# Kernel optimization log

Hardware: AMD Instinct MI355X
Metric: run time of the kernel (lower is better)

Reference implementation:

```python
import jax, jax.numpy as jnp
import numpy as np

B, T, O, H, CTX, HOR = 32, 24, 128, 512, 256, 48
MAX_STEP = 2.0


def setup_inputs() -> dict:
    key = jax.random.key(0)
    ks = jax.random.split(key, 20)
    def lin(k, out_d, in_d):
        bound = 1.0 / np.sqrt(in_d)
        kw, kb = jax.random.split(k)
        W = jax.random.uniform(kw, (out_d, in_d), jnp.float32, -bound, bound)
        b = jax.random.uniform(kb, (out_d,), jnp.float32, -bound, bound)
        return W, b
    W_emb, b_emb = lin(ks[0], H, 2)
    W_ctx, b_ctx = lin(ks[1], H, CTX)
    Wi_enc, bi_enc = lin(ks[2], 3 * H, H)
    Wh_enc, bh_enc = lin(ks[3], 3 * H, H)
    Wi_cell, bi_cell = lin(ks[4], 3 * H, H)
    Wh_cell, bh_cell = lin(ks[5], 3 * H, H)
    W1, b1 = lin(ks[6], H, H)
    W2, b2 = lin(ks[7], 2, H)
    z_ctx = jax.random.normal(ks[8], (B, CTX), jnp.float32)
    traj_hist = jax.random.uniform(ks[9], (B, T, O, 2), jnp.float32) * 10.0
    return dict(z_ctx=z_ctx, traj_hist=traj_hist,
                W_emb=W_emb, b_emb=b_emb, W_ctx=W_ctx, b_ctx=b_ctx,
                Wi_enc=Wi_enc, Wh_enc=Wh_enc, bi_enc=bi_enc, bh_enc=bh_enc,
                Wi_cell=Wi_cell, Wh_cell=Wh_cell, bi_cell=bi_cell, bh_cell=bh_cell,
                W1=W1, b1=b1, W2=W2, b2=b2, horizon=HOR)


def _gru(h, x, Wi, Wh, bi, bh):
    # PyTorch GRU gate math: gates ordered (r, z, n)
    gi = x @ Wi.T + bi  # [N, 3H]
    gh = h @ Wh.T + bh
    ir, iz, inn = jnp.split(gi, 3, axis=-1)
    hr, hz, hn = jnp.split(gh, 3, axis=-1)
    r = jax.nn.sigmoid(ir + hr)
    z = jax.nn.sigmoid(iz + hz)
    n = jnp.tanh(inn + r * hn)
    return (1.0 - z) * n + z * h


def reference(z_ctx, traj_hist, W_emb, b_emb, W_ctx, b_ctx,
              Wi_enc, Wh_enc, bi_enc, bh_enc,
              Wi_cell, Wh_cell, bi_cell, bh_cell,
              W1, b1, W2, b2, horizon):
    b, t, o, _ = traj_hist.shape
    Hd = W_emb.shape[0]
    seq = traj_hist.transpose(0, 2, 1, 3).reshape(b * o, t, 2)  # [N, t, 2]
    emb = seq @ W_emb.T + b_emb  # [N, t, H]

    h0 = jnp.zeros((b * o, Hd), traj_hist.dtype)
    def enc_step(h, x):
        return _gru(h, x, Wi_enc, Wh_enc, bi_enc, bh_enc), None
    h, _ = jax.lax.scan(enc_step, h0, emb.transpose(1, 0, 2))

    ctx = z_ctx @ W_ctx.T + b_ctx                         # [b, H]
    ctx = jnp.repeat(ctx[:, None, :], o, axis=1).reshape(b * o, Hd)
    h = h + ctx

    state0 = seq[:, -1]  # [N, 2]
    def dec_step(carry, _):
        h, state = carry
        inp = state @ W_emb.T + b_emb
        h = _gru(h, inp, Wi_cell, Wh_cell, bi_cell, bh_cell)
        d = jax.nn.gelu(h @ W1.T + b1, approximate=False) @ W2.T + b2  # [N, 2]
        d = MAX_STEP * jnp.tanh(d / MAX_STEP)
        s = state + d
        state = jnp.stack([jnp.clip(s[..., 0], -90.0, 90.0),
                           jnp.mod(s[..., 1], 360.0)], axis=-1)
        return (h, state), state
    _, outs = jax.lax.scan(dec_step, (h, state0), None, length=horizon)
    # outs: [horizon, N, 2] -> [b, horizon, o, 2]
    return outs.transpose(1, 0, 2).reshape(b, o, horizon, 2).transpose(0, 2, 1, 3)
```

## Files before the change

kernel.cpp:

```cpp
#include <hip/hip_runtime.h>
#include <hip/hip_bf16.h>
#include <math.h>

#define BB 32
#define TT 24
#define OO 128
#define HH 512
#define CTXD 256
#define HOR 48
#define NN (BB*OO)
#define G3 (3*HH)
#define KS2 16
#define TILE_U16 (KS2*512)

typedef unsigned short ushortt;
typedef __attribute__((ext_vector_type(8))) short bf16x8;
typedef __attribute__((ext_vector_type(4))) float f32x4;

__device__ __forceinline__ ushortt f2bf(float x) {
    union { float f; unsigned u; } v; v.f = x;
    unsigned r = v.u + 0x7FFF + ((v.u >> 16) & 1);
    return (ushortt)(r >> 16);
}
__device__ __forceinline__ float bf2f(ushortt b) {
    union { unsigned u; float f; } v; v.u = ((unsigned)b) << 16;
    return v.f;
}
__device__ __forceinline__ void splitbf(float x, ushortt& hi, ushortt& lo) {
    hi = f2bf(x);
    lo = f2bf(x - bf2f(hi));
}
__device__ __forceinline__ float sigm(float x) { return 1.f / (1.f + __expf(-x)); }
__device__ __forceinline__ float tanh_fast(float x) {
    float xc = fminf(fmaxf(x, -10.f), 10.f);
    float e = __expf(2.f * xc);
    return (e - 1.f) / (e + 1.f);
}

__device__ __forceinline__ void group_barrier(unsigned* cnt, unsigned target) {
    __syncthreads();
    if (threadIdx.x == 0) {
        __hip_atomic_fetch_add(cnt, 1u, __ATOMIC_RELAXED, __HIP_MEMORY_SCOPE_AGENT);
        while (__hip_atomic_load(cnt, __ATOMIC_RELAXED, __HIP_MEMORY_SCOPE_AGENT) < target)
            __builtin_amdgcn_s_sleep(2);
    }
    __syncthreads();
    asm volatile("buffer_inv sc0\n\ts_waitcnt vmcnt(0)" ::: "memory");
}


#define MLOADA(Ad, ksv) do { const unsigned ko = (unsigned)(ksv) * 512; \
  _Pragma("unroll") for (int m_ = 0; m_ < 2; m_++) { \
    Ad[m_*2+0] = *reinterpret_cast<const bf16x8*>(RAh + ao[m_] + ko); \
    Ad[m_*2+1] = *reinterpret_cast<const bf16x8*>(RAl + ao[m_] + ko); \
  } } while(0)
#define MLOADB(Bd, ksv) do { const unsigned ko = (unsigned)(ksv) * 512; \
  _Pragma("unroll") for (int g_ = 0; g_ < 3; g_++) { \
    Bd[g_*2+0] = *reinterpret_cast<const bf16x8*>(Bh + bo[g_] + ko); \
    Bd[g_*2+1] = *reinterpret_cast<const bf16x8*>(Bl + bo[g_] + ko); \
  } } while(0)
#define MMFMA(Av, Bv) do { \
  _Pragma("unroll") for (int m_ = 0; m_ < 2; m_++) \
  _Pragma("unroll") for (int g_ = 0; g_ < 3; g_++) \
    acc[m_][g_] = __builtin_amdgcn_mfma_f32_16x16x32_bf16(Av[m_*2+0], Bv[g_*2+0], acc[m_][g_], 0,0,0); \
  _Pragma("unroll") for (int m_ = 0; m_ < 2; m_++) \
  _Pragma("unroll") for (int g_ = 0; g_ < 3; g_++) \
    acc[m_][g_] = __builtin_amdgcn_mfma_f32_16x16x32_bf16(Av[m_*2+0], Bv[g_*2+1], acc[m_][g_], 0,0,0); \
  _Pragma("unroll") for (int m_ = 0; m_ < 2; m_++) \
  _Pragma("unroll") for (int g_ = 0; g_ < 3; g_++) \
    acc[m_][g_] = __builtin_amdgcn_mfma_f32_16x16x32_bf16(Av[m_*2+1], Bv[g_*2+0], acc[m_][g_], 0,0,0); \
  } while(0)

#define HLOADA(Ad, ksv) do { const unsigned ko = (unsigned)(ksv) * 512; \
  _Pragma("unroll") for (int m_ = 0; m_ < 2; m_++) { \
    Ad[m_*2+0] = *reinterpret_cast<const bf16x8*>(WAh + ao[m_] + ko); \
    Ad[m_*2+1] = *reinterpret_cast<const bf16x8*>(WAl + ao[m_] + ko); \
  } } while(0)
#define HLOADB(Bd, ksv) do { const unsigned ko = (unsigned)(ksv) * 512; \
    Bd[0] = *reinterpret_cast<const bf16x8*>(W1H + bo1 + ko); \
    Bd[1] = *reinterpret_cast<const bf16x8*>(W1L + bo1 + ko); \
  } while(0)
#define HMFMA(Av, Bv) do { \
  _Pragma("unroll") for (int m_ = 0; m_ < 2; m_++) { \
    hacc[m_] = __builtin_amdgcn_mfma_f32_16x16x32_bf16(Av[m_*2+0], Bv[0], hacc[m_], 0,0,0); \
    hacc[m_] = __builtin_amdgcn_mfma_f32_16x16x32_bf16(Av[m_*2+0], Bv[1], hacc[m_], 0,0,0); \
    hacc[m_] = __builtin_amdgcn_mfma_f32_16x16x32_bf16(Av[m_*2+1], Bv[0], hacc[m_], 0,0,0); \
  } } while(0)

__global__ __launch_bounds__(256, 4) void main_kernel(
    ushortt* Ah0, ushortt* Al0, ushortt* Ah1, ushortt* Al1,
    const ushortt* __restrict__ WheH, const ushortt* __restrict__ WheL,
    const ushortt* __restrict__ WhdH, const ushortt* __restrict__ WhdL,
    const ushortt* __restrict__ W1H,  const ushortt* __restrict__ W1L,
    const float* __restrict__ Ue, const float* __restrict__ ce,
    const float* __restrict__ Ud, const float* __restrict__ cd,
    const float* __restrict__ bhe, const float* __restrict__ bhd,
    const float* __restrict__ traj, const float* __restrict__ ctx,
    const float* __restrict__ b1v, const float* __restrict__ W2,
    const float* __restrict__ b2v, float* __restrict__ dpart,
    unsigned* bar, float* __restrict__ out)
{
    __shared__ float hbuf[128 * 20];
    __shared__ float sstate[128 * 2];
    const int mb = blockIdx.x & 31;
    const int jb = blockIdx.x >> 5;
    const int w = threadIdx.x >> 6, lane = threadIdx.x & 63;
    const int quad = lane >> 4, l15 = lane & 15;
    const int mtg = mb * 8 + w * 2;
    const int jlo = jb * 16;
    const int jcol = jlo + l15;
    unsigned* grpcnt = bar + mb * 16;
    unsigned tgt = 0;

    ushortt* bh_[2] = {Ah0, Ah1};
    ushortt* bl_[2] = {Al0, Al1};

    unsigned ao[2], bo[3], bo1;
#pragma unroll
    for (int mt = 0; mt < 2; mt++) ao[mt] = (unsigned)(mtg + mt) * TILE_U16 + lane * 8;
#pragma unroll
    for (int g = 0; g < 3; g++) bo[g] = (unsigned)(g*32 + jb) * TILE_U16 + lane * 8;
    bo1 = (unsigned)jb * TILE_U16 + lane * 8;

    const float b1r = b1v[jcol], w2a = W2[jcol], w2b = W2[HH + jcol];
    const float b20 = b2v[0], b21 = b2v[1];

    float Ur0, Ur1, Uz0, Uz1, Un0, Un1, Crr, Czz, bhn, cinn;

#pragma unroll 1
    for (int s = 0; s < TT + HOR; s++) {
        const bool enc = s < TT;
        if (s == 0 || s == TT) {
            const float* U  = enc ? Ue : Ud;
            const float* ci = enc ? ce : cd;
            const float* bh = enc ? bhe : bhd;
            Ur0 = U[jcol*2];            Ur1 = U[jcol*2+1];
            Uz0 = U[(512+jcol)*2];      Uz1 = U[(512+jcol)*2+1];
            Un0 = U[(1024+jcol)*2];     Un1 = U[(1024+jcol)*2+1];
            Crr = ci[jcol] + bh[jcol];
            Czz = ci[512+jcol] + bh[512+jcol];
            cinn = ci[1024+jcol];       bhn = bh[1024+jcol];
            if (!enc) {
                if (threadIdx.x < 128) {
                    int lrow = threadIdx.x;
                    const float* sp = traj + (((size_t)mb * TT + 23) * OO + lrow) * 2;
                    sstate[lrow*2] = sp[0]; sstate[lrow*2+1] = sp[1];
                }
                __syncthreads();
            }
        }
        const ushortt* RAh = bh_[s & 1];
        const ushortt* RAl = bl_[s & 1];
        ushortt* WAh = bh_[(s + 1) & 1];
        ushortt* WAl = bl_[(s + 1) & 1];
        const ushortt* Bh = enc ? WheH : WhdH;
        const ushortt* Bl = enc ? WheL : WhdL;

        f32x4 acc[2][3];
#pragma unroll
        for (int a = 0; a < 2; a++)
#pragma unroll
            for (int g = 0; g < 3; g++) acc[a][g] = (f32x4){0.f,0.f,0.f,0.f};

        if (s > 0) {
            bf16x8 aC[4], bC[6], aN[4], bN[6];
            MLOADA(aC, 0); MLOADB(bC, 0);
#pragma unroll 1
            for (int ks = 0; ks < 14; ks += 2) {
                MLOADA(aN, ks+1); MLOADB(bN, ks+1);
                MMFMA(aC, bC);
                MLOADA(aC, ks+2); MLOADB(bC, ks+2);
                MMFMA(aN, bN);
            }
            MLOADA(aN, 15); MLOADB(bN, 15);
            MMFMA(aC, bC);
            MMFMA(aN, bN);
        }

        float x0v[2][4], x1v[2][4];
#pragma unroll
        for (int mt = 0; mt < 2; mt++)
#pragma unroll
            for (int reg = 0; reg < 4; reg++) {
                int lrow = (w*2 + mt) * 16 + quad * 4 + reg;
                if (enc) {
                    const float* p = traj + (((size_t)mb * TT + s) * OO + lrow) * 2;
                    x0v[mt][reg] = p[0]; x1v[mt][reg] = p[1];
                } else {
                    x0v[mt][reg] = sstate[lrow*2]; x1v[mt][reg] = sstate[lrow*2+1];
                }
            }

#pragma unroll
        for (int mt = 0; mt < 2; mt++)
#pragma unroll
            for (int reg = 0; reg < 4; reg++) {
                int lrow = (w*2 + mt) * 16 + quad * 4 + reg;
                float x0 = x0v[mt][reg], x1 = x1v[mt][reg];
                float pr = acc[mt][0][reg] + fmaf(x1, Ur1, fmaf(x0, Ur0, Crr));
                float pz = acc[mt][1][reg] + fmaf(x1, Uz1, fmaf(x0, Uz0, Czz));
                float hn = acc[mt][2][reg] + bhn;
                float inn = fmaf(x1, Un1, fmaf(x0, Un0, cinn));
                float hold = (s > 0) ? hbuf[lrow * 20 + l15] : 0.f;
                float rg = sigm(pr), zg = sigm(pz);
                float nn = tanh_fast(inn + rg * hn);
                float h = (1.f - zg) * nn + zg * hold;
                if (enc && s == TT - 1)
                    h += ctx[(size_t)mb * HH + jcol];
                hbuf[lrow * 20 + l15] = h;
            }
        __syncthreads();
        {
            int fr = threadIdx.x;
            int mt8 = fr >> 5, rem = fr & 31;
            int qk = rem >> 4, r15 = rem & 15;
            const float4 v0 = *reinterpret_cast<const float4*>(&hbuf[(mt8*16 + r15) * 20 + qk * 8]);
            const float4 v1 = *reinterpret_cast<const float4*>(&hbuf[(mt8*16 + r15) * 20 + qk * 8 + 4]);
            float src[8] = {v0.x, v0.y, v0.z, v0.w, v1.x, v1.y, v1.z, v1.w};
            bf16x8 hv, lv;
#pragma unroll
            for (int q = 0; q < 8; q++) {
                ushortt hi, lo; splitbf(src[q], hi, lo);
                hv[q] = (short)hi; lv[q] = (short)lo;
            }
            int quadg = (jb & 1) * 2 + qk;
            unsigned base = (unsigned)(mb*8 + mt8) * TILE_U16 + (unsigned)(jb >> 1) * 512
                          + (unsigned)(quadg * 16 + r15) * 8;
            *reinterpret_cast<bf16x8*>(WAh + base) = hv;
            *reinterpret_cast<bf16x8*>(WAl + base) = lv;
        }

        tgt += 32;
        group_barrier(grpcnt, tgt);

        if (!enc) {
            f32x4 hacc[2];
            hacc[0] = (f32x4){0.f,0.f,0.f,0.f};
            hacc[1] = (f32x4){0.f,0.f,0.f,0.f};
            {
                bf16x8 aC[4], bC[2], aN[4], bN[2];
                HLOADA(aC, 0); HLOADB(bC, 0);
#pragma unroll 1
                for (int ks = 0; ks < 14; ks += 2) {
                    HLOADA(aN, ks+1); HLOADB(bN, ks+1);
                    HMFMA(aC, bC);
                    HLOADA(aC, ks+2); HLOADB(bC, ks+2);
                    HMFMA(aN, bN);
                }
                HLOADA(aN, 15); HLOADB(bN, 15);
                HMFMA(aC, bC);
                HMFMA(aN, bN);
            }
            float p0[2][4], p1[2][4];
#pragma unroll
            for (int mt = 0; mt < 2; mt++)
#pragma unroll
                for (int reg = 0; reg < 4; reg++) {
                    float v = hacc[mt][reg] + b1r;
                    v = 0.5f * v * (1.0f + erff(v * 0.70710678118654752440f));
                    p0[mt][reg] = v * w2a;
                    p1[mt][reg] = v * w2b;
                }
#pragma unroll
            for (int m = 1; m < 16; m <<= 1)
#pragma unroll
                for (int mt = 0; mt < 2; mt++)
#pragma unroll
                    for (int reg = 0; reg < 4; reg++) {
                        p0[mt][reg] += __shfl_xor(p0[mt][reg], m, 64);
                        p1[mt][reg] += __shfl_xor(p1[mt][reg], m, 64);
                    }
            if (l15 == 0) {
#pragma unroll
                for (int mt = 0; mt < 2; mt++)
#pragma unroll
                    for (int reg = 0; reg < 4; reg++) {
                        int lrow = (w*2 + mt) * 16 + quad * 4 + reg;
                        float* dp = dpart + ((size_t)(mb*32 + jb) * 128 + lrow) * 2;
                        dp[0] = p0[mt][reg]; dp[1] = p1[mt][reg];
                    }
            }
            tgt += 32;
            group_barrier(grpcnt, tgt);
            if (threadIdx.x < 128) {
                int lrow = threadIdx.x;
                float d0 = 0.f, d1 = 0.f;
#pragma unroll 8
                for (int j2 = 0; j2 < 32; j2++) {
                    const float* dp = dpart + ((size_t)(mb*32 + j2) * 128 + lrow) * 2;
                    d0 += dp[0]; d1 += dp[1];
                }
                d0 += b20; d1 += b21;
                d0 = 2.0f * tanhf(d0 * 0.5f);
                d1 = 2.0f * tanhf(d1 * 0.5f);
                float s0 = sstate[lrow*2] + d0;
                s0 = fminf(fmaxf(s0, -90.f), 90.f);
                float s1 = sstate[lrow*2+1] + d1;
                float rrm = fmodf(s1, 360.f);
                if (rrm < 0.f) rrm += 360.f;
                sstate[lrow*2] = s0; sstate[lrow*2+1] = rrm;
                if (jb == 0) {
                    float* op = out + (((size_t)mb * HOR + (s - TT)) * OO + lrow) * 2;
                    op[0] = s0; op[1] = rrm;
                }
            }
            __syncthreads();
        }
    }
}

__device__ __forceinline__ void pack16(const float* __restrict__ W,
                                       ushortt* __restrict__ Fh, ushortt* __restrict__ Fl,
                                       int item) {
    int n = item >> 6, rem = item & 63;
    int ks = rem >> 2, quadk = rem & 3;
    int nt = n >> 4, l15 = n & 15;
    ushortt hv[8], lv[8];
#pragma unroll
    for (int q = 0; q < 8; q++) {
        float v = W[(size_t)n * 512 + ks*32 + quadk*8 + q];
        ushortt hi, lo; splitbf(v, hi, lo);
        hv[q] = hi; lv[q] = lo;
    }
    size_t pos = ((size_t)nt * TILE_U16) + (size_t)ks * 512 + (quadk*16 + l15) * 8;
#pragma unroll
    for (int q = 0; q < 8; q++) { Fh[pos + q] = hv[q]; Fl[pos + q] = lv[q]; }
}

__global__ __launch_bounds__(256) void prep_kernel(
    const float* __restrict__ Wh_enc, const float* __restrict__ Wh_cell,
    const float* __restrict__ W1,
    const float* __restrict__ Wi_enc, const float* __restrict__ bi_enc,
    const float* __restrict__ Wi_cell, const float* __restrict__ bi_cell,
    const float* __restrict__ W_emb, const float* __restrict__ b_emb,
    const float* __restrict__ z, const float* __restrict__ Wc, const float* __restrict__ bc,
    ushortt* __restrict__ WheH, ushortt* __restrict__ WheL,
    ushortt* __restrict__ WhdH, ushortt* __restrict__ WhdL,
    ushortt* __restrict__ W1H, ushortt* __restrict__ W1L,
    float* __restrict__ Ue, float* __restrict__ ce,
    float* __restrict__ Ud, float* __restrict__ cd,
    float* __restrict__ ctx, unsigned* __restrict__ bar)
{
    int b = blockIdx.x;
    if (b < 384) {
        pack16(Wh_enc, WheH, WheL, b * 256 + threadIdx.x);
    } else if (b < 768) {
        pack16(Wh_cell, WhdH, WhdL, (b - 384) * 256 + threadIdx.x);
    } else if (b < 896) {
        pack16(W1, W1H, W1L, (b - 768) * 256 + threadIdx.x);
    } else if (b < 1664) {
        int w = threadIdx.x >> 6, lane = threadIdx.x & 63;
        int gidx = (b - 896) * 4 + w;
        int which = gidx >= G3;
        int j = gidx - which * G3;
        const float* Wi = which ? Wi_cell : Wi_enc;
        const float* bi = which ? bi_cell : bi_enc;
        float u0 = 0.f, u1 = 0.f, cc = 0.f;
#pragma unroll
        for (int i = 0; i < 8; i++) {
            int k = i * 64 + lane;
            float wv = Wi[(size_t)j * HH + k];
            u0 = fmaf(wv, W_emb[2*k],   u0);
            u1 = fmaf(wv, W_emb[2*k+1], u1);
            cc = fmaf(wv, b_emb[k],     cc);
        }
#pragma unroll
        for (int m = 1; m < 64; m <<= 1) {
            u0 += __shfl_xor(u0, m, 64);
            u1 += __shfl_xor(u1, m, 64);
            cc += __shfl_xor(cc, m, 64);
        }
        if (lane == 0) {
            float* Uo = which ? Ud : Ue;
            float* cv = which ? cd : ce;
            Uo[j*2] = u0; Uo[j*2+1] = u1; cv[j] = cc + bi[j];
        }
    } else if (b < 1728) {
        int idx = (b - 1664) * 256 + threadIdx.x;
        int bb = idx >> 9, j = idx & 511;
        float acc = bc[j];
        const float4* zp = (const float4*)(z + (size_t)bb * CTXD);
        const float4* wp = (const float4*)(Wc + (size_t)j * CTXD);
#pragma unroll 4
        for (int k = 0; k < CTXD / 4; k++) {
            float4 a = zp[k], ww = wp[k];
            acc = fmaf(a.x, ww.x, fmaf(a.y, ww.y, fmaf(a.z, ww.z, fmaf(a.w, ww.w, acc))));
        }
        ctx[idx] = acc;
    } else {
        bar[threadIdx.x] = 0u;
        bar[threadIdx.x + 256] = 0u;
    }
}

extern "C" void kernel_launch(void* const* d_in, const int* in_sizes, int n_in,
                              void* d_out, int out_size, void* d_ws, size_t ws_size,
                              hipStream_t stream) {
    const float* z_ctx   = (const float*)d_in[0];
    const float* traj    = (const float*)d_in[1];
    const float* W_emb   = (const float*)d_in[2];
    const float* b_emb   = (const float*)d_in[3];
    const float* W_ctx   = (const float*)d_in[4];
    const float* b_ctx   = (const float*)d_in[5];
    const float* Wi_enc  = (const float*)d_in[6];
    const float* Wh_enc  = (const float*)d_in[7];
    const float* bi_enc  = (const float*)d_in[8];
    const float* bh_enc  = (const float*)d_in[9];
    const float* Wi_cell = (const float*)d_in[10];
    const float* Wh_cell = (const float*)d_in[11];
    const float* bi_cell = (const float*)d_in[12];
    const float* bh_cell = (const float*)d_in[13];
    const float* W1      = (const float*)d_in[14];
    const float* b1      = (const float*)d_in[15];
    const float* W2      = (const float*)d_in[16];
    const float* b2      = (const float*)d_in[17];
    float* out = (float*)d_out;

    char* ws = (char*)d_ws;
    size_t off = 0;
    auto alloc = [&](size_t bytes) { void* p = ws + off; off += (bytes + 255) & ~(size_t)255; return p; };
    const size_t hfrag  = (size_t)256 * TILE_U16 * 2;
    const size_t wfrag  = (size_t)96  * TILE_U16 * 2;
    const size_t w1frag = (size_t)32  * TILE_U16 * 2;
    ushortt* Ah0 = (ushortt*)alloc(hfrag);
    ushortt* Al0 = (ushortt*)alloc(hfrag);
    ushortt* Ah1 = (ushortt*)alloc(hfrag);
    ushortt* Al1 = (ushortt*)alloc(hfrag);
    ushortt* WheH = (ushortt*)alloc(wfrag);
    ushortt* WheL = (ushortt*)alloc(wfrag);
    ushortt* WhdH = (ushortt*)alloc(wfrag);
    ushortt* WhdL = (ushortt*)alloc(wfrag);
    ushortt* W1H  = (ushortt*)alloc(w1frag);
    ushortt* W1L  = (ushortt*)alloc(w1frag);
    float* Ue   = (float*)alloc((size_t)G3 * 2 * 4);
    float* ce   = (float*)alloc((size_t)G3 * 4);
    float* Ud   = (float*)alloc((size_t)G3 * 2 * 4);
    float* cd   = (float*)alloc((size_t)G3 * 4);
    float* ctxb = (float*)alloc((size_t)BB * HH * 4);
    float* dpart = (float*)alloc((size_t)32 * 32 * 128 * 2 * 4);
    unsigned* bar = (unsigned*)alloc(512 * 4);

    prep_kernel<<<1729, 256, 0, stream>>>(Wh_enc, Wh_cell, W1,
                                          Wi_enc, bi_enc, Wi_cell, bi_cell,
                                          W_emb, b_emb, z_ctx, W_ctx, b_ctx,
                                          WheH, WheL, WhdH, WhdL, W1H, W1L,
                                          Ue, ce, Ud, cd, ctxb, bar);

    main_kernel<<<1024, 256, 0, stream>>>(Ah0, Al0, Ah1, Al1,
                                          WheH, WheL, WhdH, WhdL, W1H, W1L,
                                          Ue, ce, Ud, cd, bh_enc, bh_cell,
                                          traj, ctxb, b1, W2, b2,
                                          dpart, bar, out);
}
```

Before: 4.205 ms.

## Merge column-block pairs into 512-thread blocks to halve group-barrier participants

Each workgroup now has 8 waves covering 32 hidden columns instead of 4 waves covering 16. The grid shrinks from 1024 to 512 blocks, and each per-batch group barrier waits on 16 arrivals instead of 32. The shared h buffer is widened to hold both column halves, and the bf16 hi/lo writeback now writes one contiguous 512-element tile chunk per block. The aim is to cut the global-barrier latency that dominates the 72 serial recurrent steps. The cost is larger blocks with more register and LDS pressure per block, and an intra-block __syncthreads spanning 8 waves.

Result: faster. 3.716 ms (-11.6%).

```diff
diff --git a/kernel.cpp b/kernel.cpp
--- a/kernel.cpp
+++ b/kernel.cpp
@@ -87,7 +87,7 @@
     hacc[m_] = __builtin_amdgcn_mfma_f32_16x16x32_bf16(Av[m_*2+1], Bv[0], hacc[m_], 0,0,0); \
   } } while(0)
 
-__global__ __launch_bounds__(256, 4) void main_kernel(
+__global__ __launch_bounds__(512, 4) void main_kernel(
     ushortt* Ah0, ushortt* Al0, ushortt* Ah1, ushortt* Al1,
     const ushortt* __restrict__ WheH, const ushortt* __restrict__ WheL,
     const ushortt* __restrict__ WhdH, const ushortt* __restrict__ WhdL,
@@ -100,15 +100,18 @@
     const float* __restrict__ b2v, float* __restrict__ dpart,
     unsigned* bar, float* __restrict__ out)
 {
-    __shared__ float hbuf[128 * 20];
+    __shared__ float hbuf[128 * 36];
     __shared__ float sstate[128 * 2];
     const int mb = blockIdx.x & 31;
     const int jb = blockIdx.x >> 5;
-    const int w = threadIdx.x >> 6, lane = threadIdx.x & 63;
+    const int w = threadIdx.x >> 6;
+    const int lane = threadIdx.x & 63;
     const int quad = lane >> 4, l15 = lane & 15;
-    const int mtg = mb * 8 + w * 2;
-    const int jlo = jb * 16;
-    const int jcol = jlo + l15;
+    const int mp = w & 3;
+    const int jh = w >> 2;
+    const int mtg = mb * 8 + mp * 2;
+    const int jlo = jb * 32;
+    const int jcol = jlo + jh * 16 + l15;
     unsigned* grpcnt = bar + mb * 16;
     unsigned tgt = 0;
 
@@ -119,8 +122,8 @@
 #pragma unroll
     for (int mt = 0; mt < 2; mt++) ao[mt] = (unsigned)(mtg + mt) * TILE_U16 + lane * 8;
 #pragma unroll
-    for (int g = 0; g < 3; g++) bo[g] = (unsigned)(g*32 + jb) * TILE_U16 + lane * 8;
-    bo1 = (unsigned)jb * TILE_U16 + lane * 8;
+    for (int g = 0; g < 3; g++) bo[g] = (unsigned)(g*32 + jb*2 + jh) * TILE_U16 + lane * 8;
+    bo1 = (unsigned)(jb*2 + jh) * TILE_U16 + lane * 8;
 
     const float b1r = b1v[jcol], w2a = W2[jcol], w2b = W2[HH + jcol];
     const float b20 = b2v[0], b21 = b2v[1];
@@ -182,7 +185,7 @@
         for (int mt = 0; mt < 2; mt++)
 #pragma unroll
             for (int reg = 0; reg < 4; reg++) {
-                int lrow = (w*2 + mt) * 16 + quad * 4 + reg;
+                int lrow = (mp*2 + mt) * 16 + quad * 4 + reg;
                 if (enc) {
                     const float* p = traj + (((size_t)mb * TT + s) * OO + lrow) * 2;
                     x0v[mt][reg] = p[0]; x1v[mt][reg] = p[1];
@@ -195,27 +198,28 @@
         for (int mt = 0; mt < 2; mt++)
 #pragma unroll
             for (int reg = 0; reg < 4; reg++) {
-                int lrow = (w*2 + mt) * 16 + quad * 4 + reg;
+                int lrow = (mp*2 + mt) * 16 + quad * 4 + reg;
                 float x0 = x0v[mt][reg], x1 = x1v[mt][reg];
                 float pr = acc[mt][0][reg] + fmaf(x1, Ur1, fmaf(x0, Ur0, Crr));
                 float pz = acc[mt][1][reg] + fmaf(x1, Uz1, fmaf(x0, Uz0, Czz));
                 float hn = acc[mt][2][reg] + bhn;
                 float inn = fmaf(x1, Un1, fmaf(x0, Un0, cinn));
-                float hold = (s > 0) ? hbuf[lrow * 20 + l15] : 0.f;
+                float hold = (s > 0) ? hbuf[lrow * 36 + jh*16 + l15] : 0.f;
                 float rg = sigm(pr), zg = sigm(pz);
                 float nn = tanh_fast(inn + rg * hn);
                 float h = (1.f - zg) * nn + zg * hold;
                 if (enc && s == TT - 1)
                     h += ctx[(size_t)mb * HH + jcol];
-                hbuf[lrow * 20 + l15] = h;
+                hbuf[lrow * 36 + jh*16 + l15] = h;
             }
         __syncthreads();
         {
             int fr = threadIdx.x;
-            int mt8 = fr >> 5, rem = fr & 31;
-            int qk = rem >> 4, r15 = rem & 15;
-            const float4 v0 = *reinterpret_cast<const float4*>(&hbuf[(mt8*16 + r15) * 20 + qk * 8]);
-            const float4 v1 = *reinterpret_cast<const float4*>(&hbuf[(mt8*16 + r15) * 20 + qk * 8 + 4]);
+            int mt8 = fr >> 6, fl = fr & 63;
+            int qk = fl >> 4, r15 = fl & 15;
+            int rloc = mt8 * 16 + r15;
+            const float4 v0 = *reinterpret_cast<const float4*>(&hbuf[rloc * 36 + qk * 8]);
+            const float4 v1 = *reinterpret_cast<const float4*>(&hbuf[rloc * 36 + qk * 8 + 4]);
             float src[8] = {v0.x, v0.y, v0.z, v0.w, v1.x, v1.y, v1.z, v1.w};
             bf16x8 hv, lv;
 #pragma unroll
@@ -223,14 +227,12 @@
                 ushortt hi, lo; splitbf(src[q], hi, lo);
                 hv[q] = (short)hi; lv[q] = (short)lo;
             }
-            int quadg = (jb & 1) * 2 + qk;
-            unsigned base = (unsigned)(mb*8 + mt8) * TILE_U16 + (unsigned)(jb >> 1) * 512
-                          + (unsigned)(quadg * 16 + r15) * 8;
+            unsigned base = (unsigned)(mb*8 + mt8) * TILE_U16 + (unsigned)jb * 512 + fl * 8;
             *reinterpret_cast<bf16x8*>(WAh + base) = hv;
             *reinterpret_cast<bf16x8*>(WAl + base) = lv;
         }
 
-        tgt += 32;
+        tgt += 16;
         group_barrier(grpcnt, tgt);
 
         if (!enc) {
@@ -275,12 +277,12 @@
                 for (int mt = 0; mt < 2; mt++)
 #pragma unroll
                     for (int reg = 0; reg < 4; reg++) {
-                        int lrow = (w*2 + mt) * 16 + quad * 4 + reg;
-                        float* dp = dpart + ((size_t)(mb*32 + jb) * 128 + lrow) * 2;
+                        int lrow = (mp*2 + mt) * 16 + quad * 4 + reg;
+                        float* dp = dpart + ((size_t)(mb*32 + jb*2 + jh) * 128 + lrow) * 2;
                         dp[0] = p0[mt][reg]; dp[1] = p1[mt][reg];
                     }
             }
-            tgt += 32;
+            tgt += 16;
             group_barrier(grpcnt, tgt);
             if (threadIdx.x < 128) {
                 int lrow = threadIdx.x;
@@ -446,9 +448,9 @@
                                           WheH, WheL, WhdH, WhdL, W1H, W1L,
                                           Ue, ce, Ud, cd, ctxb, bar);
 
-    main_kernel<<<1024, 256, 0, stream>>>(Ah0, Al0, Ah1, Al1,
-                                          WheH, WheL, WhdH, WhdL, W1H, W1L,
-                                          Ue, ce, Ud, cd, bh_enc, bh_cell,
-                                          traj, ctxb, b1, W2, b2,
-                                          dpart, bar, out);
-}
+    main_kernel<<<512, 512, 0, stream>>>(Ah0, Al0, Ah1, Al1,
+                                         WheH, WheL, WhdH, WhdL, W1H, W1L,
+                                         Ue, ce, Ud, cd, bh_enc, bh_cell,
+                                         traj, ctxb, b1, W2, b2,
+                                         dpart, bar, out);
+}
```
